# Kernel optimization log

Measured on AMD Instinct MI355X. Metric: run time of the kernel, lower is better.

## Reference

```python
import jax, jax.numpy as jnp
import numpy as np

N = 50000
E = 800000
IN_DIM = 256
HID = 64
HEADS = 4
OUT_DIM = 40
NEG_SLOPE = 0.2


def _gatv2_conv(x, src, dst, Wl, bl, Wr, br, att, bias, concat):
    """PyG GATv2Conv (share_weights=False, eval mode, no attn dropout).
    src -> message source nodes, dst -> target nodes (softmax over dst)."""
    H, C = att.shape
    n = x.shape[0]
    xl = (x @ Wl + bl).reshape(n, H, C)  # source/message transform (lin_l)
    xr = (x @ Wr + br).reshape(n, H, C)  # target transform (lin_r)
    # per-edge logits: [E, H]
    s = xl[src] + xr[dst]                                  # [E,H,C]
    e = jnp.einsum('ehc,hc->eh', jax.nn.leaky_relu(s, NEG_SLOPE), att)
    # segment softmax over incoming edges of each target node
    m = jax.ops.segment_max(e, dst, num_segments=n)        # [N,H]
    m = jnp.where(jnp.isfinite(m), m, 0.0)                 # empty segments
    ex = jnp.exp(e - m[dst])
    denom = jax.ops.segment_sum(ex, dst, num_segments=n)   # [N,H]
    alpha = ex / (denom[dst] + 1e-16)                      # [E,H]
    out = jax.ops.segment_sum(alpha[:, :, None] * xl[src], dst, num_segments=n)
    if concat:
        out = out.reshape(n, H * C)
    else:
        out = out.mean(axis=1)
    return out + bias


def setup_inputs() -> dict:
    key = jax.random.key(0)
    ks = jax.random.split(key, 12)
    sc = 0.05
    return {
        'x': jax.random.normal(ks[0], (N, IN_DIM), jnp.float32),
        'src': jax.random.randint(ks[1], (E,), 0, N, jnp.int32),
        'dst': jax.random.randint(ks[2], (E,), 0, N, jnp.int32),
        'Wl1': jax.random.normal(ks[3], (IN_DIM, HEADS * HID), jnp.float32) * sc,
        'bl1': jnp.zeros((HEADS * HID,), jnp.float32),
        'Wr1': jax.random.normal(ks[4], (IN_DIM, HEADS * HID), jnp.float32) * sc,
        'br1': jnp.zeros((HEADS * HID,), jnp.float32),
        'att1': jax.random.normal(ks[5], (HEADS, HID), jnp.float32) * sc,
        'bias1': jnp.zeros((HEADS * HID,), jnp.float32),
        'Wl2': jax.random.normal(ks[6], (HEADS * HID, HEADS * HID), jnp.float32) * sc,
        'bl2': jnp.zeros((HEADS * HID,), jnp.float32),
        'Wr2': jax.random.normal(ks[7], (HEADS * HID, HEADS * HID), jnp.float32) * sc,
        'br2': jnp.zeros((HEADS * HID,), jnp.float32),
        'att2': jax.random.normal(ks[8], (HEADS, HID), jnp.float32) * sc,
        'bias2': jnp.zeros((HID,), jnp.float32),
        'Wc': jax.random.normal(ks[9], (HID, OUT_DIM), jnp.float32) * sc,
        'bc': jnp.zeros((OUT_DIM,), jnp.float32),
    }


def reference(x, src, dst, Wl1, bl1, Wr1, br1, att1, bias1,
              Wl2, bl2, Wr2, br2, att2, bias2, Wc, bc):
    h = _gatv2_conv(x, src, dst, Wl1, bl1, Wr1, br1, att1, bias1, concat=True)
    h = jax.nn.relu(h)  # dropout p applied only in training; eval -> identity
    h = _gatv2_conv(h, src, dst, Wl2, bl2, Wr2, br2, att2, bias2, concat=False)
    h = jax.nn.relu(h)
    return h @ Wc + bc  # [N, OUT_DIM]
```

## Files before the change

### kernel.cpp

```cpp
#include <hip/hip_runtime.h>
#include <hip/hip_bf16.h>
#include <math.h>


#define IN_DIM 256
#define HIDHC 256
#define HID 64
#define OUT_DIM 40

using half8  = __attribute__((ext_vector_type(8))) _Float16;
using half4  = __attribute__((ext_vector_type(4))) _Float16;
using half2v = __attribute__((ext_vector_type(2))) _Float16;
using f32x4  = __attribute__((ext_vector_type(4))) float;

__device__ __forceinline__ void gload16(const void* g, void* l) {
    __builtin_amdgcn_global_load_lds(
        (const __attribute__((address_space(1))) void*)g,
        (__attribute__((address_space(3))) void*)l, 16, 0, 0);
}


__global__ void edge_hist(const int* __restrict__ dst, int* __restrict__ deg, int E) {
    int i = blockIdx.x * blockDim.x + threadIdx.x;
    if (i < E) atomicAdd(&deg[dst[i]], 1);
}

__global__ void deg_block_reduce(const int* __restrict__ deg, int* __restrict__ bsum, int n) {
    int i = blockIdx.x * 256 + threadIdx.x;
    int v = (i < n) ? deg[i] : 0;
    #pragma unroll
    for (int off = 32; off; off >>= 1) v += __shfl_xor(v, off, 64);
    __shared__ int ws[4];
    int lane = threadIdx.x & 63, wid = threadIdx.x >> 6;
    if (lane == 0) ws[wid] = v;
    __syncthreads();
    if (threadIdx.x == 0) bsum[blockIdx.x] = ws[0] + ws[1] + ws[2] + ws[3];
}

__global__ void scan_bsums(const int* __restrict__ bsum, int* __restrict__ bpre, int nb) {
    __shared__ int s[256];
    int tid = threadIdx.x;
    int orig = (tid < nb) ? bsum[tid] : 0;
    s[tid] = orig;
    __syncthreads();
    #pragma unroll
    for (int off = 1; off < 256; off <<= 1) {
        int t = (tid >= off) ? s[tid - off] : 0;
        __syncthreads();
        s[tid] += t;
        __syncthreads();
    }
    if (tid < nb) bpre[tid] = s[tid] - orig;
}

__global__ void deg_scan_apply(const int* __restrict__ deg, const int* __restrict__ bpre,
                               int* __restrict__ offsets, int* __restrict__ cursor, int n) {
    int i = blockIdx.x * 256 + threadIdx.x;
    int lane = threadIdx.x & 63, wid = threadIdx.x >> 6;
    int v = (i < n) ? deg[i] : 0;
    int inc = v;
    #pragma unroll
    for (int off = 1; off < 64; off <<= 1) {
        int t = __shfl_up(inc, off, 64);
        if (lane >= off) inc += t;
    }
    __shared__ int ws[4];
    if (lane == 63) ws[wid] = inc;
    __syncthreads();
    int add = bpre[blockIdx.x];
    for (int w = 0; w < wid; ++w) add += ws[w];
    int incl = inc + add;
    if (i < n) { offsets[i + 1] = incl; cursor[i] = incl - v; }
    if (i == 0) offsets[0] = 0;
}

__global__ void edge_scatter(const int* __restrict__ src, const int* __restrict__ dst,
                             int* __restrict__ cursor, int* __restrict__ csr_src, int E) {
    int i = blockIdx.x * blockDim.x + threadIdx.x;
    if (i < E) {
        int p = atomicAdd(&cursor[dst[i]], 1);
        csr_src[p] = src[i];
    }
}


__global__ void cvt_f16(const float* __restrict__ in, _Float16* __restrict__ out, int n4) {
    int i = blockIdx.x * blockDim.x + threadIdx.x;
    if (i >= n4) return;
    float4 v = ((const float4*)in)[i];
    half4 h = { (_Float16)v.x, (_Float16)v.y, (_Float16)v.z, (_Float16)v.w };
    ((half4*)out)[i] = h;
}

__global__ void prep_weights(const float* __restrict__ W0, const float* __restrict__ W1,
                             const float* __restrict__ W2, const float* __restrict__ W3,
                             _Float16* __restrict__ T) {
    const float* Wsel = (blockIdx.y == 0) ? W0 : (blockIdx.y == 1) ? W1
                      : (blockIdx.y == 2) ? W2 : W3;
    int k = blockIdx.x, nn = threadIdx.x;
    float v = Wsel[k * 256 + nn];
    T[(size_t)blockIdx.y * 65536 + (size_t)nn * 256 + k] = (_Float16)v;
}


__global__ __launch_bounds__(256) void gemm2_mfma(
    const _Float16* __restrict__ A,
    const _Float16* __restrict__ W0, const float* __restrict__ b0, _Float16* __restrict__ C0,
    const _Float16* __restrict__ W1, const float* __restrict__ b1, _Float16* __restrict__ C1,
    int M)
{
    __shared__ __align__(16) _Float16 sA[2][4096], sB[2][4096];

    const _Float16* W   = blockIdx.z ? W1 : W0;
    const float*    bias= blockIdx.z ? b1 : b0;
    _Float16*       C   = blockIdx.z ? C1 : C0;

    int tid = threadIdx.x;
    int bm = blockIdx.x * 128;
    int bn = blockIdx.y * 128;

    int lane = tid & 63, w = tid >> 6;
    int r = lane & 15, q = lane >> 4;
    int m0 = (w >> 1) * 64, n0 = (w & 1) * 64;

    int arow[2], brow[2], kgo[2], lds[2];
    #pragma unroll
    for (int i = 0; i < 2; ++i) {
        int g = tid + 256 * i;
        kgo[i] = (g >> 7) * 8;
        int row = g & 127;
        arow[i] = min(bm + row, M - 1);
        brow[i] = bn + row;
        lds[i] = g * 8;
    }

    f32x4 acc[4][4];
    #pragma unroll
    for (int i = 0; i < 4; ++i)
        #pragma unroll
        for (int j = 0; j < 4; ++j) acc[i][j] = (f32x4)0.f;

    #pragma unroll
    for (int i = 0; i < 2; ++i) {
        gload16(A + (size_t)arow[i] * 256 + kgo[i], &sA[0][lds[i]]);
        gload16(W + (size_t)brow[i] * 256 + kgo[i], &sB[0][lds[i]]);
    }
    __builtin_amdgcn_s_waitcnt(0);
    __syncthreads();

    #pragma unroll 1
    for (int kt = 0; kt < 8; ++kt) {
        int buf = kt & 1;
        if (kt < 7) {
            int k0 = (kt + 1) * 32;
            #pragma unroll
            for (int i = 0; i < 2; ++i) {
                gload16(A + (size_t)arow[i] * 256 + k0 + kgo[i], &sA[buf ^ 1][lds[i]]);
                gload16(W + (size_t)brow[i] * 256 + k0 + kgo[i], &sB[buf ^ 1][lds[i]]);
            }
        }
        half8 a[4], b[4];
        #pragma unroll
        for (int i = 0; i < 4; ++i) {
            a[i] = *(const half8*)(&sA[buf][(q * 128 + m0 + i * 16 + r) * 8]);
            b[i] = *(const half8*)(&sB[buf][(q * 128 + n0 + i * 16 + r) * 8]);
        }
        #pragma unroll
        for (int i = 0; i < 4; ++i)
            #pragma unroll
            for (int j = 0; j < 4; ++j)
                acc[i][j] = __builtin_amdgcn_mfma_f32_16x16x32_f16(a[i], b[j], acc[i][j], 0, 0, 0);
        __builtin_amdgcn_s_waitcnt(0);
        __syncthreads();
    }

    float bv[4];
    #pragma unroll
    for (int j = 0; j < 4; ++j) bv[j] = bias[bn + n0 + j * 16 + r];
    #pragma unroll
    for (int i = 0; i < 4; ++i) {
        #pragma unroll
        for (int reg = 0; reg < 4; ++reg) {
            int row = bm + m0 + i * 16 + q * 4 + reg;
            if (row < M) {
                #pragma unroll
                for (int j = 0; j < 4; ++j)
                    C[(size_t)row * 256 + bn + n0 + j * 16 + r] =
                        (_Float16)(acc[i][j][reg] + bv[j]);
            }
        }
    }
}


__global__ __launch_bounds__(256) void gat_node(
    const _Float16* __restrict__ xl, const _Float16* __restrict__ xr,
    const float* __restrict__ att, const float* __restrict__ bias,
    const int* __restrict__ offsets, const int* __restrict__ csr_src,
    void* __restrict__ out0, int n, int mode)
{
    int wid = threadIdx.x >> 6;
    int node = (blockIdx.x << 2) + wid;
    if (node >= n) return;
    int lane = threadIdx.x & 63;
    int H = lane >> 5;
    int p = lane & 31;

    const half2v c02 = { (_Float16)0.2f, (_Float16)0.2f };

    half8 xrh = *(const half8*)(xr + (size_t)node * HIDHC + p * 8);
    half2v xr01 = __builtin_shufflevector(xrh, xrh, 0, 1);
    half2v xr23 = __builtin_shufflevector(xrh, xrh, 2, 3);
    half2v xr45 = __builtin_shufflevector(xrh, xrh, 4, 5);
    half2v xr67 = __builtin_shufflevector(xrh, xrh, 6, 7);

    float4 af0 = *(const float4*)(att + p * 8);
    float4 af1 = *(const float4*)(att + p * 8 + 4);
    half2v at01 = { (_Float16)af0.x, (_Float16)af0.y };
    half2v at23 = { (_Float16)af0.z, (_Float16)af0.w };
    half2v at45 = { (_Float16)af1.x, (_Float16)af1.y };
    half2v at67 = { (_Float16)af1.z, (_Float16)af1.w };

    float acc[8];
    #pragma unroll
    for (int k = 0; k < 8; ++k) acc[k] = 0.f;
    float d = 0.f;

    int j0 = __builtin_amdgcn_readfirstlane(offsets[node]);
    int j1 = __builtin_amdgcn_readfirstlane(offsets[node + 1]);

    int j = j0;
    for (; j + 2 <= j1; j += 2) {
        int s0 = __builtin_amdgcn_readfirstlane(csr_src[j]);
        int s1 = __builtin_amdgcn_readfirstlane(csr_src[j + 1]);
        int s = H ? s1 : s0;
        half8 h = *(const half8*)(xl + (size_t)s * HIDHC + p * 8);
        half2v h01 = __builtin_shufflevector(h, h, 0, 1);
        half2v h23 = __builtin_shufflevector(h, h, 2, 3);
        half2v h45 = __builtin_shufflevector(h, h, 4, 5);
        half2v h67 = __builtin_shufflevector(h, h, 6, 7);
        half2v s01 = h01 + xr01, s23 = h23 + xr23, s45 = h45 + xr45, s67 = h67 + xr67;
        half2v l01 = __builtin_elementwise_max(s01, s01 * c02);
        half2v l23 = __builtin_elementwise_max(s23, s23 * c02);
        half2v l45 = __builtin_elementwise_max(s45, s45 * c02);
        half2v l67 = __builtin_elementwise_max(s67, s67 * c02);
        float e = __builtin_amdgcn_fdot2(l01, at01, 0.f, false);
        e = __builtin_amdgcn_fdot2(l23, at23, e, false);
        e = __builtin_amdgcn_fdot2(l45, at45, e, false);
        e = __builtin_amdgcn_fdot2(l67, at67, e, false);
        e += __shfl_xor(e, 1);
        e += __shfl_xor(e, 2);
        e += __shfl_xor(e, 4);
        float pw = __expf(e);
        d += pw;
        #pragma unroll
        for (int k = 0; k < 8; ++k) acc[k] = fmaf(pw, (float)h[k], acc[k]);
    }
    if (j < j1) {
        int s0 = __builtin_amdgcn_readfirstlane(csr_src[j]);
        half8 h = *(const half8*)(xl + (size_t)s0 * HIDHC + p * 8);
        half2v h01 = __builtin_shufflevector(h, h, 0, 1);
        half2v h23 = __builtin_shufflevector(h, h, 2, 3);
        half2v h45 = __builtin_shufflevector(h, h, 4, 5);
        half2v h67 = __builtin_shufflevector(h, h, 6, 7);
        half2v s01 = h01 + xr01, s23 = h23 + xr23, s45 = h45 + xr45, s67 = h67 + xr67;
        half2v l01 = __builtin_elementwise_max(s01, s01 * c02);
        half2v l23 = __builtin_elementwise_max(s23, s23 * c02);
        half2v l45 = __builtin_elementwise_max(s45, s45 * c02);
        half2v l67 = __builtin_elementwise_max(s67, s67 * c02);
        float e = __builtin_amdgcn_fdot2(l01, at01, 0.f, false);
        e = __builtin_amdgcn_fdot2(l23, at23, e, false);
        e = __builtin_amdgcn_fdot2(l45, at45, e, false);
        e = __builtin_amdgcn_fdot2(l67, at67, e, false);
        e += __shfl_xor(e, 1);
        e += __shfl_xor(e, 2);
        e += __shfl_xor(e, 4);
        float pw = (H == 0) ? __expf(e) : 0.f;
        d += pw;
        #pragma unroll
        for (int k = 0; k < 8; ++k) acc[k] = fmaf(pw, (float)h[k], acc[k]);
    }

    d += __shfl_xor(d, 32);
    #pragma unroll
    for (int k = 0; k < 8; ++k) acc[k] += __shfl_xor(acc[k], 32);

    float inv = 1.f / (d + 1e-16f);
    float o[8];
    #pragma unroll
    for (int k = 0; k < 8; ++k) o[k] = acc[k] * inv;

    if (mode == 0) {
        if (H == 0) {
            float4 b0 = *(const float4*)(bias + p * 8);
            float4 b1 = *(const float4*)(bias + p * 8 + 4);
            float bb[8] = { b0.x, b0.y, b0.z, b0.w, b1.x, b1.y, b1.z, b1.w };
            half8 hh;
            #pragma unroll
            for (int k = 0; k < 8; ++k) hh[k] = (_Float16)fmaxf(o[k] + bb[k], 0.f);
            *(half8*)((_Float16*)out0 + (size_t)node * HIDHC + p * 8) = hh;
        }
    } else {
        #pragma unroll
        for (int k = 0; k < 8; ++k) {
            o[k] += __shfl_xor(o[k], 8);
            o[k] += __shfl_xor(o[k], 16);
        }
        if (lane < 8) {
            float4 b0 = *(const float4*)(bias + p * 8);
            float4 b1 = *(const float4*)(bias + p * 8 + 4);
            float bb[8] = { b0.x, b0.y, b0.z, b0.w, b1.x, b1.y, b1.z, b1.w };
            float4 o0, o1;
            o0.x = fmaxf(o[0] * 0.25f + bb[0], 0.f);
            o0.y = fmaxf(o[1] * 0.25f + bb[1], 0.f);
            o0.z = fmaxf(o[2] * 0.25f + bb[2], 0.f);
            o0.w = fmaxf(o[3] * 0.25f + bb[3], 0.f);
            o1.x = fmaxf(o[4] * 0.25f + bb[4], 0.f);
            o1.y = fmaxf(o[5] * 0.25f + bb[5], 0.f);
            o1.z = fmaxf(o[6] * 0.25f + bb[6], 0.f);
            o1.w = fmaxf(o[7] * 0.25f + bb[7], 0.f);
            float* dst = (float*)out0 + (size_t)node * HID + p * 8;
            *(float4*)dst = o0;
            *(float4*)(dst + 4) = o1;
        }
    }
}


__global__ __launch_bounds__(256) void final_linear(
    const float* __restrict__ h2, const float* __restrict__ Wc,
    const float* __restrict__ bc, float* __restrict__ out, int n)
{
    __shared__ float Ws[HID * OUT_DIM];
    __shared__ float bs[OUT_DIM];
    __shared__ float hs[64][HID + 1];

    for (int i = threadIdx.x; i < HID * OUT_DIM; i += 256) Ws[i] = Wc[i];
    if (threadIdx.x < OUT_DIM) bs[threadIdx.x] = bc[threadIdx.x];

    int n0 = blockIdx.x * 64;
    for (int i = threadIdx.x; i < 64 * HID; i += 256) {
        int r = i >> 6, c = i & 63;
        int node = n0 + r;
        hs[r][c] = (node < n) ? h2[(size_t)node * HID + c] : 0.f;
    }
    __syncthreads();

    for (int idx = threadIdx.x; idx < 64 * OUT_DIM; idx += 256) {
        int r = idx / OUT_DIM, o = idx % OUT_DIM;
        int node = n0 + r;
        if (node < n) {
            float s = bs[o];
            #pragma unroll
            for (int c = 0; c < HID; ++c) s = fmaf(hs[r][c], Ws[c * OUT_DIM + o], s);
            out[(size_t)node * OUT_DIM + o] = s;
        }
    }
}


extern "C" void kernel_launch(void* const* d_in, const int* in_sizes, int n_in,
                              void* d_out, int out_size, void* d_ws, size_t ws_size,
                              hipStream_t stream) {
    const int N = in_sizes[0] / IN_DIM;
    const int E = in_sizes[1];

    const float* x    = (const float*)d_in[0];
    const int*   src  = (const int*)d_in[1];
    const int*   dst  = (const int*)d_in[2];
    const float* Wl1  = (const float*)d_in[3];
    const float* bl1  = (const float*)d_in[4];
    const float* Wr1  = (const float*)d_in[5];
    const float* br1  = (const float*)d_in[6];
    const float* att1 = (const float*)d_in[7];
    const float* bias1= (const float*)d_in[8];
    const float* Wl2  = (const float*)d_in[9];
    const float* bl2  = (const float*)d_in[10];
    const float* Wr2  = (const float*)d_in[11];
    const float* br2  = (const float*)d_in[12];
    const float* att2 = (const float*)d_in[13];
    const float* bias2= (const float*)d_in[14];
    const float* Wc   = (const float*)d_in[15];
    const float* bc   = (const float*)d_in[16];

    char* ws = (char*)d_ws;
    size_t off = 0;
    _Float16* xlh = (_Float16*)(ws + off); off += (size_t)N * HIDHC * 2;
    _Float16* xrh = (_Float16*)(ws + off); off += (size_t)N * HIDHC * 2;
    _Float16* Af  = (_Float16*)(ws + off); off += (size_t)N * HIDHC * 2;
    float*    h2  = (float*)(ws + off);    off += (size_t)N * HID * 4;
    _Float16* Wt  = (_Float16*)(ws + off); off += (size_t)4 * 65536 * 2;
    int* deg     = (int*)(ws + off); off += (size_t)N * 4;
    int* offsets = (int*)(ws + off); off += (size_t)(N + 1) * 4;
    int* cursor  = (int*)(ws + off); off += (size_t)N * 4;
    int* csr     = (int*)(ws + off); off += (size_t)E * 4;
    int* bsum    = (int*)(ws + off); off += 256 * 4;
    int* bpre    = (int*)(ws + off); off += 256 * 4;

    const int NB = (N + 255) / 256;

    hipMemsetAsync(deg, 0, (size_t)N * 4, stream);
    edge_hist<<<(E + 255) / 256, 256, 0, stream>>>(dst, deg, E);
    deg_block_reduce<<<NB, 256, 0, stream>>>(deg, bsum, N);
    scan_bsums<<<1, 256, 0, stream>>>(bsum, bpre, NB);
    deg_scan_apply<<<NB, 256, 0, stream>>>(deg, bpre, offsets, cursor, N);
    edge_scatter<<<(E + 255) / 256, 256, 0, stream>>>(src, dst, cursor, csr, E);
    prep_weights<<<dim3(256, 4), 256, 0, stream>>>(Wl1, Wr1, Wl2, Wr2, Wt);
    cvt_f16<<<(N * HIDHC / 4 + 255) / 256, 256, 0, stream>>>(x, Af, N * HIDHC / 4);

    const int KW = 65536;
    dim3 gg((N + 127) / 128, 2, 2);
    gemm2_mfma<<<gg, 256, 0, stream>>>(Af,
        Wt + 0 * KW, bl1, xlh,
        Wt + 1 * KW, br1, xrh, N);
    gat_node<<<(N + 3) / 4, 256, 0, stream>>>(xlh, xrh, att1, bias1, offsets, csr,
                                              (void*)Af, N, 0);
    gemm2_mfma<<<gg, 256, 0, stream>>>(Af,
        Wt + 2 * KW, bl2, xlh,
        Wt + 3 * KW, br2, xrh, N);
    gat_node<<<(N + 3) / 4, 256, 0, stream>>>(xlh, xrh, att2, bias2, offsets, csr,
                                              (void*)h2, N, 1);
    final_linear<<<(N + 63) / 64, 256, 0, stream>>>(h2, Wc, bc, (float*)d_out, N);
}
```

Baseline: 459.6 us.

## Fuse dual GEMM into one 512-thread block and prefetch gathers in GAT aggregation

The GEMM now computes both lin_l and lin_r outputs across the full 256 columns in one 512-thread block. Each A tile is loaded once and reused by eight waves, instead of being reloaded by four separate blocks. The gat_node kernel loads up to 64 neighbor indices into lanes with one coalesced read and then broadcasts them with shuffles. It also software-pipelines the xl row gathers two edges ahead to hide memory latency. Costs are higher register pressure from the doubled accumulators and a larger LDS footprint per block, which may reduce occupancy.

New measurement: 451.4 us. Within noise of the previous version (-1.8%).

```diff
diff --git a/kernel.cpp b/kernel.cpp
--- a/kernel.cpp
+++ b/kernel.cpp
@@ -103,47 +103,53 @@
 }
 
 
-__global__ __launch_bounds__(256) void gemm2_mfma(
+__global__ __launch_bounds__(512, 2) void gemm_dual(
     const _Float16* __restrict__ A,
     const _Float16* __restrict__ W0, const float* __restrict__ b0, _Float16* __restrict__ C0,
     const _Float16* __restrict__ W1, const float* __restrict__ b1, _Float16* __restrict__ C1,
     int M)
 {
-    __shared__ __align__(16) _Float16 sA[2][4096], sB[2][4096];
-
-    const _Float16* W   = blockIdx.z ? W1 : W0;
-    const float*    bias= blockIdx.z ? b1 : b0;
-    _Float16*       C   = blockIdx.z ? C1 : C0;
+    __shared__ __align__(16) _Float16 sA[2][4096];
+    __shared__ __align__(16) _Float16 sW[2][2][8192];
 
     int tid = threadIdx.x;
     int bm = blockIdx.x * 128;
-    int bn = blockIdx.y * 128;
 
     int lane = tid & 63, w = tid >> 6;
+    int z = w >> 2, wq = w & 3;
     int r = lane & 15, q = lane >> 4;
-    int m0 = (w >> 1) * 64, n0 = (w & 1) * 64;
-
-    int arow[2], brow[2], kgo[2], lds[2];
-    #pragma unroll
-    for (int i = 0; i < 2; ++i) {
-        int g = tid + 256 * i;
-        kgo[i] = (g >> 7) * 8;
-        int row = g & 127;
-        arow[i] = min(bm + row, M - 1);
-        brow[i] = bn + row;
-        lds[i] = g * 8;
-    }
-
-    f32x4 acc[4][4];
-    #pragma unroll
-    for (int i = 0; i < 4; ++i)
-        #pragma unroll
-        for (int j = 0; j < 4; ++j) acc[i][j] = (f32x4)0.f;
-
-    #pragma unroll
-    for (int i = 0; i < 2; ++i) {
-        gload16(A + (size_t)arow[i] * 256 + kgo[i], &sA[0][lds[i]]);
-        gload16(W + (size_t)brow[i] * 256 + kgo[i], &sB[0][lds[i]]);
+    int m0 = (wq >> 1) * 64, n0 = (wq & 1) * 64;
+
+    int akg  = (tid >> 7) * 8;
+    int arow = min(bm + (tid & 127), M - 1);
+    int alds = tid * 8;
+
+    int wzi[4], wro[4], wkg[4], wld[4];
+    #pragma unroll
+    for (int i = 0; i < 4; ++i) {
+        int g2 = tid + 512 * i;
+        wzi[i] = g2 >> 10;
+        int rem = g2 & 1023;
+        int kgroup = rem >> 8;
+        int row = rem & 255;
+        wro[i] = row;
+        wkg[i] = kgroup * 8;
+        wld[i] = (kgroup * 256 + row) * 8;
+    }
+
+    f32x4 acc[2][4][4];
+    #pragma unroll
+    for (int nt = 0; nt < 2; ++nt)
+        #pragma unroll
+        for (int i = 0; i < 4; ++i)
+            #pragma unroll
+            for (int j = 0; j < 4; ++j) acc[nt][i][j] = (f32x4)0.f;
+
+    gload16(A + (size_t)arow * 256 + akg, &sA[0][alds]);
+    #pragma unroll
+    for (int i = 0; i < 4; ++i) {
+        const _Float16* wp = wzi[i] ? W1 : W0;
+        gload16(wp + (size_t)wro[i] * 256 + wkg[i], &sW[0][wzi[i]][wld[i]]);
     }
     __builtin_amdgcn_s_waitcnt(0);
     __syncthreads();
@@ -153,40 +159,52 @@
         int buf = kt & 1;
         if (kt < 7) {
             int k0 = (kt + 1) * 32;
-            #pragma unroll
-            for (int i = 0; i < 2; ++i) {
-                gload16(A + (size_t)arow[i] * 256 + k0 + kgo[i], &sA[buf ^ 1][lds[i]]);
-                gload16(W + (size_t)brow[i] * 256 + k0 + kgo[i], &sB[buf ^ 1][lds[i]]);
+            gload16(A + (size_t)arow * 256 + k0 + akg, &sA[buf ^ 1][alds]);
+            #pragma unroll
+            for (int i = 0; i < 4; ++i) {
+                const _Float16* wp = wzi[i] ? W1 : W0;
+                gload16(wp + (size_t)wro[i] * 256 + k0 + wkg[i], &sW[buf ^ 1][wzi[i]][wld[i]]);
             }
         }
-        half8 a[4], b[4];
-        #pragma unroll
-        for (int i = 0; i < 4; ++i) {
+        half8 a[4];
+        #pragma unroll
+        for (int i = 0; i < 4; ++i)
             a[i] = *(const half8*)(&sA[buf][(q * 128 + m0 + i * 16 + r) * 8]);
-            b[i] = *(const half8*)(&sB[buf][(q * 128 + n0 + i * 16 + r) * 8]);
-        }
-        #pragma unroll
-        for (int i = 0; i < 4; ++i)
+        #pragma unroll
+        for (int nt = 0; nt < 2; ++nt) {
+            half8 b[4];
             #pragma unroll
             for (int j = 0; j < 4; ++j)
-                acc[i][j] = __builtin_amdgcn_mfma_f32_16x16x32_f16(a[i], b[j], acc[i][j], 0, 0, 0);
+                b[j] = *(const half8*)(&sW[buf][z][(q * 256 + nt * 128 + n0 + j * 16 + r) * 8]);
+            #pragma unroll
+            for (int i = 0; i < 4; ++i)
+                #pragma unroll
+                for (int j = 0; j < 4; ++j)
+                    acc[nt][i][j] = __builtin_amdgcn_mfma_f32_16x16x32_f16(a[i], b[j], acc[nt][i][j], 0, 0, 0);
+        }
         __builtin_amdgcn_s_waitcnt(0);
         __syncthreads();
     }
 
-    float bv[4];
-    #pragma unroll
-    for (int j = 0; j < 4; ++j) bv[j] = bias[bn + n0 + j * 16 + r];
-    #pragma unroll
-    for (int i = 0; i < 4; ++i) {
-        #pragma unroll
-        for (int reg = 0; reg < 4; ++reg) {
-            int row = bm + m0 + i * 16 + q * 4 + reg;
-            if (row < M) {
-                #pragma unroll
-                for (int j = 0; j < 4; ++j)
-                    C[(size_t)row * 256 + bn + n0 + j * 16 + r] =
-                        (_Float16)(acc[i][j][reg] + bv[j]);
+    const float* bias = z ? b1 : b0;
+    _Float16*    C    = z ? C1 : C0;
+
+    #pragma unroll
+    for (int nt = 0; nt < 2; ++nt) {
+        float bv[4];
+        #pragma unroll
+        for (int j = 0; j < 4; ++j) bv[j] = bias[nt * 128 + n0 + j * 16 + r];
+        #pragma unroll
+        for (int i = 0; i < 4; ++i) {
+            #pragma unroll
+            for (int reg = 0; reg < 4; ++reg) {
+                int orow = bm + m0 + i * 16 + q * 4 + reg;
+                if (orow < M) {
+                    #pragma unroll
+                    for (int j = 0; j < 4; ++j)
+                        C[(size_t)orow * 256 + nt * 128 + n0 + j * 16 + r] =
+                            (_Float16)(acc[nt][i][j][reg] + bv[j]);
+                }
             }
         }
     }
@@ -226,15 +244,7 @@
     for (int k = 0; k < 8; ++k) acc[k] = 0.f;
     float d = 0.f;
 
-    int j0 = __builtin_amdgcn_readfirstlane(offsets[node]);
-    int j1 = __builtin_amdgcn_readfirstlane(offsets[node + 1]);
-
-    int j = j0;
-    for (; j + 2 <= j1; j += 2) {
-        int s0 = __builtin_amdgcn_readfirstlane(csr_src[j]);
-        int s1 = __builtin_amdgcn_readfirstlane(csr_src[j + 1]);
-        int s = H ? s1 : s0;
-        half8 h = *(const half8*)(xl + (size_t)s * HIDHC + p * 8);
+    auto edge_compute = [&](half8 h) {
         half2v h01 = __builtin_shufflevector(h, h, 0, 1);
         half2v h23 = __builtin_shufflevector(h, h, 2, 3);
         half2v h45 = __builtin_shufflevector(h, h, 4, 5);
@@ -255,6 +265,46 @@
         d += pw;
         #pragma unroll
         for (int k = 0; k < 8; ++k) acc[k] = fmaf(pw, (float)h[k], acc[k]);
+    };
+
+    int j0 = __builtin_amdgcn_readfirstlane(offsets[node]);
+    int j1 = __builtin_amdgcn_readfirstlane(offsets[node + 1]);
+    int deg = j1 - j0;
+
+    int fast = min(deg, 64);
+    int npf = fast >> 1;
+    int idxv = 0;
+    if (lane < fast) idxv = csr_src[j0 + lane];
+
+    half8 hA, hB;
+    if (npf > 0) { int s = __shfl(idxv, 0 + H, 64); hA = *(const half8*)(xl + (size_t)s * HIDHC + p * 8); }
+    if (npf > 1) { int s = __shfl(idxv, 2 + H, 64); hB = *(const half8*)(xl + (size_t)s * HIDHC + p * 8); }
+    int t = 0;
+    for (; t + 4 <= npf; t += 2) {
+        half8 ha = hA, hb = hB;
+        { int s = __shfl(idxv, (t + 2) * 2 + H, 64); hA = *(const half8*)(xl + (size_t)s * HIDHC + p * 8); }
+        { int s = __shfl(idxv, (t + 3) * 2 + H, 64); hB = *(const half8*)(xl + (size_t)s * HIDHC + p * 8); }
+        edge_compute(ha);
+        edge_compute(hb);
+    }
+    if (t + 2 <= npf) {
+        half8 ha = hA, hb = hB;
+        if (t + 2 < npf) { int s = __shfl(idxv, (t + 2) * 2 + H, 64); hA = *(const half8*)(xl + (size_t)s * HIDHC + p * 8); }
+        edge_compute(ha);
+        edge_compute(hb);
+        t += 2;
+    }
+    if (t < npf) {
+        edge_compute(hA);
+    }
+
+    int j = j0 + (npf << 1);
+    for (; j + 2 <= j1; j += 2) {
+        int s0 = __builtin_amdgcn_readfirstlane(csr_src[j]);
+        int s1 = __builtin_amdgcn_readfirstlane(csr_src[j + 1]);
+        int s = H ? s1 : s0;
+        half8 h = *(const half8*)(xl + (size_t)s * HIDHC + p * 8);
+        edge_compute(h);
     }
     if (j < j1) {
         int s0 = __builtin_amdgcn_readfirstlane(csr_src[j]);
@@ -409,13 +459,13 @@
     cvt_f16<<<(N * HIDHC / 4 + 255) / 256, 256, 0, stream>>>(x, Af, N * HIDHC / 4);
 
     const int KW = 65536;
-    dim3 gg((N + 127) / 128, 2, 2);
-    gemm2_mfma<<<gg, 256, 0, stream>>>(Af,
+    const int GB = (N + 127) / 128;
+    gemm_dual<<<GB, 512, 0, stream>>>(Af,
         Wt + 0 * KW, bl1, xlh,
         Wt + 1 * KW, br1, xrh, N);
     gat_node<<<(N + 3) / 4, 256, 0, stream>>>(xlh, xrh, att1, bias1, offsets, csr,
                                               (void*)Af, N, 0);
-    gemm2_mfma<<<gg, 256, 0, stream>>>(Af,
+    gemm_dual<<<GB, 512, 0, stream>>>(Af,
         Wt + 2 * KW, bl2, xlh,
         Wt + 3 * KW, br2, xrh, N);
     gat_node<<<(N + 3) / 4, 256, 0, stream>>>(xlh, xrh, att2, bias2, offsets, csr,
```
